# Performance work log

Hardware: AMD Instinct MI355X
Metric: run time of the kernel (lower is better)

## Reference

```python
import jax, jax.numpy as jnp
import numpy as np

BATCH = 8192
FEATURES = 8192
INITIAL_SPARSITY_RATE = 0.5


def setup_inputs() -> dict:
    key = jax.random.key(0)
    k1, _ = jax.random.split(key)
    inputs = jax.random.normal(k1, (BATCH, FEATURES), dtype=jnp.float32)
    # trainable scalar weight, shape (1,), constant-initialized
    sparsity_rate = jnp.full((1,), INITIAL_SPARSITY_RATE, dtype=jnp.float32)
    return {"inputs": inputs, "sparsity_rate": sparsity_rate}


def reference(inputs, sparsity_rate):
    # inputs: [B, F]; sparsity_rate: [1]
    n = inputs.shape[-1]
    # descending sort along feature axis
    sorted_desc = -jnp.sort(-inputs, axis=-1)
    # per-call threshold index (integer cast, non-differentiable like TF's tf.cast)
    rate = jnp.clip(sparsity_rate[0], 0.0, 1.0)
    idx = jax.lax.stop_gradient((rate * jnp.float32(n)).astype(jnp.int32))
    thresh = jnp.take(sorted_desc, idx, axis=-1)           # [B]: value at rank `idx`
    max_in = jnp.max(inputs, axis=-1)                      # [B]
    t_r = max_in - thresh                                  # [B]
    # relu-masked weights: relu(x + t_r - max) == relu(x - thresh)
    w_t = jax.nn.relu(inputs + t_r[:, None] - max_in[:, None])
    weighted_exp = w_t * jnp.exp(inputs)                   # [B, F]
    sum_we = jnp.sum(weighted_exp, axis=-1, keepdims=True)
    return weighted_exp / sum_we
```

## Files before the change

### kernel.cpp

```cpp
#include <hip/hip_runtime.h>

#define ROWS 8192
#define COLS 8192
#define TPB  256
#define EPT  32
#define VPT  8

__device__ __forceinline__ unsigned f2k(float x) {
    unsigned u = __float_as_uint(x);
    return (u & 0x80000000u) ? ~u : (u | 0x80000000u);
}
__device__ __forceinline__ float k2f(unsigned k) {
    unsigned u = (k & 0x80000000u) ? (k & 0x7FFFFFFFu) : ~k;
    return __uint_as_float(u);
}

__global__ __launch_bounds__(TPB, 4)
void rsoftmax_kernel(const float* __restrict__ in,
                     const float* __restrict__ rate_p,
                     float* __restrict__ out)
{
    const int t   = threadIdx.x;
    const int row = blockIdx.x;
    const float4* in4  = (const float4*)(in  + (size_t)row * COLS);
    float4*       out4 = (float4*)      (out + (size_t)row * COLS);

    unsigned key[EPT];
    #pragma unroll
    for (int j = 0; j < VPT; ++j) {
        float4 v = in4[t + j * TPB];
        key[4*j+0] = f2k(v.x);
        key[4*j+1] = f2k(v.y);
        key[4*j+2] = f2k(v.z);
        key[4*j+3] = f2k(v.w);
    }

    float rate = rate_p[0];
    rate = fminf(fmaxf(rate, 0.0f), 1.0f);
    int idx = (int)(rate * (float)COLS);
    if (idx > COLS - 1) idx = COLS - 1;
    if (idx < 0) idx = 0;

    __shared__ unsigned sHist[256];
    __shared__ unsigned sScan[256];
    __shared__ unsigned sK, sPfx;
    __shared__ float    sW[4];
    __shared__ float    sInv;

    if (t == 0) { sK = (unsigned)(idx + 1); sPfx = 0u; }
    __syncthreads();

    #pragma unroll
    for (int pass = 0; pass < 4; ++pass) {
        const int      s      = 24 - 8 * pass;
        const unsigned himask = (pass == 0) ? 0u : (0xFFFFFFFFu << (s + 8));

        sHist[t] = 0u;
        __syncthreads();
        const unsigned pfx = sPfx;
        const unsigned kk  = sK;

        #pragma unroll
        for (int j = 0; j < EPT; ++j) {
            if (((key[j] ^ pfx) & himask) == 0u)
                atomicAdd(&sHist[(key[j] >> s) & 0xFFu], 1u);
        }
        __syncthreads();

        sScan[t] = sHist[t];
        __syncthreads();
        #pragma unroll
        for (int off = 1; off < 256; off <<= 1) {
            unsigned v = (t + off < 256) ? sScan[t + off] : 0u;
            __syncthreads();
            sScan[t] += v;
            __syncthreads();
        }

        unsigned st = sScan[t];
        unsigned sn = (t == 255) ? 0u : sScan[t + 1];
        if (st >= kk && sn < kk) {
            sPfx = pfx | ((unsigned)t << s);
            sK   = kk - sn;
        }
        __syncthreads();
    }

    const float thr = k2f(sPfx);

    float lsum = 0.0f;
    #pragma unroll
    for (int j = 0; j < EPT; ++j) {
        float x = k2f(key[j]);
        float w = fmaxf(x - thr, 0.0f);
        lsum += w * __expf(x);
    }
    #pragma unroll
    for (int off = 32; off > 0; off >>= 1)
        lsum += __shfl_down(lsum, off, 64);
    if ((t & 63) == 0) sW[t >> 6] = lsum;
    __syncthreads();
    if (t == 0) sInv = 1.0f / (sW[0] + sW[1] + sW[2] + sW[3]);
    __syncthreads();
    const float inv = sInv;

    #pragma unroll
    for (int j = 0; j < VPT; ++j) {
        float4 o;
        float x0 = k2f(key[4*j+0]); o.x = fmaxf(x0 - thr, 0.0f) * __expf(x0) * inv;
        float x1 = k2f(key[4*j+1]); o.y = fmaxf(x1 - thr, 0.0f) * __expf(x1) * inv;
        float x2 = k2f(key[4*j+2]); o.z = fmaxf(x2 - thr, 0.0f) * __expf(x2) * inv;
        float x3 = k2f(key[4*j+3]); o.w = fmaxf(x3 - thr, 0.0f) * __expf(x3) * inv;
        out4[t + j * TPB] = o;
    }
}

extern "C" void kernel_launch(void* const* d_in, const int* in_sizes, int n_in,
                              void* d_out, int out_size, void* d_ws, size_t ws_size,
                              hipStream_t stream)
{
    const float* in   = (const float*)d_in[0];
    const float* rate = (const float*)d_in[1];
    float*       out  = (float*)d_out;
    rsoftmax_kernel<<<dim3(ROWS), dim3(TPB), 0, stream>>>(in, rate, out);
}
```

Measured before the change: 465.2 us.

## Replace four-pass radix select with coarse histogram plus candidate binary search

The kernel now stages row keys in shared memory (32 KB per block) and builds a single 1024-bin histogram of the top 10 key bits, replacing four 8-bit radix passes with their Hillis-Steele scans. The bin holding the threshold is found with a wave-shuffle scan. Keys in that bin are then compacted into a candidate list and binary-searched by one wave, with a full-row fallback when the list would overflow. The weighted exponentials are stored back into shared memory so the output pass does not recompute exp. The large shared footprint may reduce occupancy compared with the register-held design, and the binary search runs serially on one wave.

Measured after the change: 493.9 us. 6.2% more time.

```diff
diff --git a/kernel.cpp b/kernel.cpp
--- a/kernel.cpp
+++ b/kernel.cpp
@@ -3,8 +3,10 @@
 #define ROWS 8192
 #define COLS 8192
 #define TPB  256
-#define EPT  32
 #define VPT  8
+#define NBINS 1024
+#define SHIFT 22
+#define CAND_CAP 1024
 
 __device__ __forceinline__ unsigned f2k(float x) {
     unsigned u = __float_as_uint(x);
@@ -20,97 +22,159 @@
                      const float* __restrict__ rate_p,
                      float* __restrict__ out)
 {
-    const int t   = threadIdx.x;
-    const int row = blockIdx.x;
-    const float4* in4  = (const float4*)(in  + (size_t)row * COLS);
-    float4*       out4 = (float4*)      (out + (size_t)row * COLS);
+    const int t    = threadIdx.x;
+    const int lane = t & 63;
+    const int wv   = t >> 6;
+    const int row  = blockIdx.x;
 
-    unsigned key[EPT];
-    #pragma unroll
-    for (int j = 0; j < VPT; ++j) {
-        float4 v = in4[t + j * TPB];
-        key[4*j+0] = f2k(v.x);
-        key[4*j+1] = f2k(v.y);
-        key[4*j+2] = f2k(v.z);
-        key[4*j+3] = f2k(v.w);
-    }
+    __shared__ __align__(16) unsigned sKeys[COLS];
+    __shared__ __align__(16) unsigned sHist[NBINS];
+    __shared__ unsigned sWaveTot[4];
+    __shared__ unsigned sBin, sR, sC, sNc, sThrKey;
+    __shared__ float    sRed[4];
+    unsigned* sCand = sHist;
 
     float rate = rate_p[0];
     rate = fminf(fmaxf(rate, 0.0f), 1.0f);
     int idx = (int)(rate * (float)COLS);
     if (idx > COLS - 1) idx = COLS - 1;
-    if (idx < 0) idx = 0;
+    const unsigned k = (unsigned)(idx + 1);
 
-    __shared__ unsigned sHist[256];
-    __shared__ unsigned sScan[256];
-    __shared__ unsigned sK, sPfx;
-    __shared__ float    sW[4];
-    __shared__ float    sInv;
-
-    if (t == 0) { sK = (unsigned)(idx + 1); sPfx = 0u; }
+    ((uint4*)sHist)[t] = make_uint4(0u, 0u, 0u, 0u);
+    if (t == 0) sNc = 0u;
     __syncthreads();
 
+    const float4* in4 = (const float4*)(in + (size_t)row * COLS);
     #pragma unroll
-    for (int pass = 0; pass < 4; ++pass) {
-        const int      s      = 24 - 8 * pass;
-        const unsigned himask = (pass == 0) ? 0u : (0xFFFFFFFFu << (s + 8));
+    for (int j = 0; j < VPT; ++j) {
+        float4 v = in4[t + j * TPB];
+        unsigned k0 = f2k(v.x), k1 = f2k(v.y), k2 = f2k(v.z), k3 = f2k(v.w);
+        ((uint4*)sKeys)[t + j * TPB] = make_uint4(k0, k1, k2, k3);
+        atomicAdd(&sHist[k0 >> SHIFT], 1u);
+        atomicAdd(&sHist[k1 >> SHIFT], 1u);
+        atomicAdd(&sHist[k2 >> SHIFT], 1u);
+        atomicAdd(&sHist[k3 >> SHIFT], 1u);
+    }
+    __syncthreads();
 
-        sHist[t] = 0u;
-        __syncthreads();
-        const unsigned pfx = sPfx;
-        const unsigned kk  = sK;
+    uint4 h4 = ((uint4*)sHist)[t];
+    unsigned L = h4.x + h4.y + h4.z + h4.w;
+    unsigned W = L;
+    #pragma unroll
+    for (int off = 1; off < 64; off <<= 1) {
+        unsigned o = __shfl(W, lane + off, 64);
+        W += (lane + off < 64) ? o : 0u;
+    }
+    if (lane == 0) sWaveTot[wv] = W;
+    __syncthreads();
+    unsigned above = W - L;
+    #pragma unroll
+    for (int w = 0; w < 4; ++w)
+        if (w > wv) above += sWaveTot[w];
+    {
+        unsigned hh[4] = {h4.x, h4.y, h4.z, h4.w};
+        unsigned nxt = above;
+        #pragma unroll
+        for (int j = 3; j >= 0; --j) {
+            unsigned cur = nxt + hh[j];
+            if (cur >= k && nxt < k) {
+                sBin = (unsigned)(4 * t + j);
+                sR   = k - nxt;
+                sC   = hh[j];
+            }
+            nxt = cur;
+        }
+    }
+    __syncthreads();
 
+    const unsigned bin = sBin;
+    const unsigned C   = sC;
+    const unsigned lo0 = bin << SHIFT;
+
+    if (C <= CAND_CAP) {
         #pragma unroll
-        for (int j = 0; j < EPT; ++j) {
-            if (((key[j] ^ pfx) & himask) == 0u)
-                atomicAdd(&sHist[(key[j] >> s) & 0xFFu], 1u);
+        for (int j = 0; j < VPT; ++j) {
+            uint4 kk = ((uint4*)sKeys)[t + j * TPB];
+            unsigned ka[4] = {kk.x, kk.y, kk.z, kk.w};
+            #pragma unroll
+            for (int q = 0; q < 4; ++q) {
+                if ((ka[q] >> SHIFT) == bin) {
+                    unsigned pos = atomicAdd(&sNc, 1u);
+                    sCand[pos] = ka[q];
+                }
+            }
         }
         __syncthreads();
-
-        sScan[t] = sHist[t];
+        if (wv == 0) {
+            unsigned lo = lo0, hi = lo0 | ((1u << SHIFT) - 1u);
+            const unsigned r = sR;
+            while (lo < hi) {
+                unsigned mid = lo + ((hi - lo) >> 1) + 1u;
+                unsigned c = 0;
+                for (unsigned i = (unsigned)lane; i < C; i += 64u)
+                    c += (sCand[i] >= mid) ? 1u : 0u;
+                #pragma unroll
+                for (int off = 32; off > 0; off >>= 1)
+                    c += __shfl_xor(c, off, 64);
+                if (c >= r) lo = mid; else hi = mid - 1u;
+            }
+            if (lane == 0) sThrKey = lo;
+        }
         __syncthreads();
-        #pragma unroll
-        for (int off = 1; off < 256; off <<= 1) {
-            unsigned v = (t + off < 256) ? sScan[t + off] : 0u;
+    } else {
+        unsigned lo = lo0, hi = lo0 | ((1u << SHIFT) - 1u);
+        while (lo < hi) {
+            unsigned mid = lo + ((hi - lo) >> 1) + 1u;
+            unsigned c = 0;
+            #pragma unroll
+            for (int j = 0; j < VPT; ++j) {
+                uint4 kk = ((uint4*)sKeys)[t + j * TPB];
+                c += (kk.x >= mid) + (kk.y >= mid) + (kk.z >= mid) + (kk.w >= mid);
+            }
+            #pragma unroll
+            for (int off = 32; off > 0; off >>= 1)
+                c += __shfl_xor(c, off, 64);
+            if (lane == 0) sWaveTot[wv] = c;
             __syncthreads();
-            sScan[t] += v;
+            c = sWaveTot[0] + sWaveTot[1] + sWaveTot[2] + sWaveTot[3];
+            if (c >= k) lo = mid; else hi = mid - 1u;
             __syncthreads();
         }
-
-        unsigned st = sScan[t];
-        unsigned sn = (t == 255) ? 0u : sScan[t + 1];
-        if (st >= kk && sn < kk) {
-            sPfx = pfx | ((unsigned)t << s);
-            sK   = kk - sn;
-        }
+        if (t == 0) sThrKey = lo;
         __syncthreads();
     }
 
-    const float thr = k2f(sPfx);
-
+    const float thr = k2f(sThrKey);
     float lsum = 0.0f;
     #pragma unroll
-    for (int j = 0; j < EPT; ++j) {
-        float x = k2f(key[j]);
-        float w = fmaxf(x - thr, 0.0f);
-        lsum += w * __expf(x);
+    for (int j = 0; j < VPT; ++j) {
+        uint4 kk = ((uint4*)sKeys)[t + j * TPB];
+        float x0 = k2f(kk.x), x1 = k2f(kk.y), x2 = k2f(kk.z), x3 = k2f(kk.w);
+        float p0 = fmaxf(x0 - thr, 0.0f) * __expf(x0);
+        float p1 = fmaxf(x1 - thr, 0.0f) * __expf(x1);
+        float p2 = fmaxf(x2 - thr, 0.0f) * __expf(x2);
+        float p3 = fmaxf(x3 - thr, 0.0f) * __expf(x3);
+        lsum += (p0 + p1) + (p2 + p3);
+        ((uint4*)sKeys)[t + j * TPB] =
+            make_uint4(__float_as_uint(p0), __float_as_uint(p1),
+                       __float_as_uint(p2), __float_as_uint(p3));
     }
     #pragma unroll
     for (int off = 32; off > 0; off >>= 1)
-        lsum += __shfl_down(lsum, off, 64);
-    if ((t & 63) == 0) sW[t >> 6] = lsum;
+        lsum += __shfl_xor(lsum, off, 64);
+    if (lane == 0) sRed[wv] = lsum;
     __syncthreads();
-    if (t == 0) sInv = 1.0f / (sW[0] + sW[1] + sW[2] + sW[3]);
-    __syncthreads();
-    const float inv = sInv;
+    const float inv = 1.0f / (sRed[0] + sRed[1] + sRed[2] + sRed[3]);
 
+    float4* out4 = (float4*)(out + (size_t)row * COLS);
     #pragma unroll
     for (int j = 0; j < VPT; ++j) {
+        uint4 p4 = ((uint4*)sKeys)[t + j * TPB];
         float4 o;
-        float x0 = k2f(key[4*j+0]); o.x = fmaxf(x0 - thr, 0.0f) * __expf(x0) * inv;
-        float x1 = k2f(key[4*j+1]); o.y = fmaxf(x1 - thr, 0.0f) * __expf(x1) * inv;
-        float x2 = k2f(key[4*j+2]); o.z = fmaxf(x2 - thr, 0.0f) * __expf(x2) * inv;
-        float x3 = k2f(key[4*j+3]); o.w = fmaxf(x3 - thr, 0.0f) * __expf(x3) * inv;
+        o.x = __uint_as_float(p4.x) * inv;
+        o.y = __uint_as_float(p4.y) * inv;
+        o.z = __uint_as_float(p4.z) * inv;
+        o.w = __uint_as_float(p4.w) * inv;
         out4[t + j * TPB] = o;
     }
 }
```
